# Performance work log

Hardware: AMD Instinct MI355X
Metric: run time of the kernel (lower is better)

The kernel has to match this reference:

```python
import jax, jax.numpy as jnp
import numpy as np

B, T, C = 2, 1024, 2048
NH, NKV = 16, 4
HD = C // NH          # 128
NUM_REP = NH // NKV   # 4


def _apply_rotation(x, angles):
    # x: (B, T, nh, hd); angles: (T, hd//2). Equivalent to the per-pair 2x2
    # rotation matmuls in the torch code: [x0', x1'] = [[cos,-sin],[sin,cos]] @ [x0, x1]
    Bx, Tx, nh, hd = x.shape
    xp = x.reshape(Bx, Tx, nh, hd // 2, 2)
    cos = jnp.cos(angles)[None, :, None, :]  # (1, T, 1, hd//2)
    sin = jnp.sin(angles)[None, :, None, :]
    x0, x1 = xp[..., 0], xp[..., 1]
    rot = jnp.stack([cos * x0 - sin * x1, sin * x0 + cos * x1], axis=-1)
    return rot.reshape(Bx, Tx, nh, hd)


def setup_inputs() -> dict:
    key = jax.random.key(0)
    ks = jax.random.split(key, 5)
    x = jax.random.normal(ks[0], (B, T, C), dtype=jnp.float32)
    # standard RoPE angle table: pos * 10000^(-2i/hd), shape (T, hd//2)
    inv_freq = 1.0 / (10000.0 ** (jnp.arange(0, HD, 2, dtype=jnp.float32) / HD))
    angles = jnp.arange(T, dtype=jnp.float32)[:, None] * inv_freq[None, :]
    s = 0.02
    wq = jax.random.normal(ks[1], (C, C), dtype=jnp.float32) * s
    wk = jax.random.normal(ks[2], (C, NKV * HD), dtype=jnp.float32) * s
    wv = jax.random.normal(ks[3], (C, NKV * HD), dtype=jnp.float32) * s
    wo = jax.random.normal(ks[4], (C, C), dtype=jnp.float32) * s
    return {"x": x, "angles": angles, "wq": wq, "wk": wk, "wv": wv, "wo": wo}


def reference(x, angles, wq, wk, wv, wo):
    Bx, Tx, Cx = x.shape
    q = (x @ wq).reshape(Bx, Tx, NH, HD)
    k = (x @ wk).reshape(Bx, Tx, NKV, HD)
    v = (x @ wv).reshape(Bx, Tx, NKV, HD)
    q = _apply_rotation(q, angles)
    k = _apply_rotation(k, angles)
    q = q.transpose(0, 2, 1, 3)  # (B, nh, T, hd)
    k = k.transpose(0, 2, 1, 3)  # (B, nkv, T, hd)
    v = v.transpose(0, 2, 1, 3)
    if NKV != 1:
        # torch .repeat tiles kv heads: query head h uses kv head h % NKV
        k = jnp.tile(k, (1, NUM_REP, 1, 1))
        v = jnp.tile(v, (1, NUM_REP, 1, 1))
    # Faithful quirks of the source: scores = K @ Q^T (keys on rows), NO 1/sqrt(hd) scale
    scores = jnp.einsum('bhkd,bhqd->bhkq', k, q)  # (B, nh, T, T)
    mask = jnp.triu(jnp.full((Tx, Tx), -jnp.inf, dtype=scores.dtype), k=1)
    scores = scores + mask
    w = jax.nn.softmax(scores, axis=-1)
    out = jnp.einsum('bhij,bhjd->bhid', w, v)   # (B, nh, T, hd)
    out = out.transpose(0, 2, 1, 3).reshape(Bx, Tx, Cx)
    return out @ wo
```

## Files before the change

kernel.cpp:

```cpp
#include <hip/hip_runtime.h>
#include <hip/hip_bf16.h>
#include <math.h>

#define BB 2
#define TT 1024
#define CC 2048
#define NH 16
#define NKV 4
#define HD 128
#define MROWS 2048
#define QKVN 3072
#define KOFF 2048
#define VOFF 2560

typedef unsigned short u16;
typedef unsigned int   u32;
typedef _Float16 f16;
typedef _Float16 f16x8 __attribute__((ext_vector_type(8)));
typedef short    s16x8 __attribute__((ext_vector_type(8)));
typedef float    f32x4 __attribute__((ext_vector_type(4)));

__device__ __forceinline__ u16 f2h(float f) {
    union { f16 h; u16 u; } x; x.h = (f16)f; return x.u;
}
__device__ __forceinline__ float h2f(u16 u) {
    union { u16 u; f16 h; } x; x.u = u; return (float)x.h;
}

#define GLDS(gp, lp) __builtin_amdgcn_global_load_lds( \
    (const __attribute__((address_space(1))) u32*)(gp), \
    (__attribute__((address_space(3))) u32*)(lp), 16, 0, 0)

__device__ __forceinline__ void wT_tile(const float* __restrict__ src,
                                        u16* __restrict__ Wt, int Nsrc,
                                        int row_off, int idx, int t,
                                        float tile[32][33]) {
    const int k0 = (idx & 63) * 32;
    const int n0 = (idx >> 6) * 32;
    const int r = t >> 3, c4 = (t & 7) * 4;
    float4 v = *(const float4*)&src[(size_t)(k0 + r) * Nsrc + n0 + c4];
    tile[r][c4 + 0] = v.x; tile[r][c4 + 1] = v.y;
    tile[r][c4 + 2] = v.z; tile[r][c4 + 3] = v.w;
    __syncthreads();
    ushort4 o;
    o.x = f2h(tile[c4 + 0][r]); o.y = f2h(tile[c4 + 1][r]);
    o.z = f2h(tile[c4 + 2][r]); o.w = f2h(tile[c4 + 3][r]);
    *(ushort4*)&Wt[(size_t)(row_off + n0 + r) * 2048 + k0 + c4] = o;
}

__global__ __launch_bounds__(256) void prep(const float* __restrict__ x,
                                            const float* __restrict__ wq,
                                            const float* __restrict__ wk,
                                            const float* __restrict__ wv,
                                            const float* __restrict__ wo,
                                            const float* __restrict__ angles,
                                            u16* __restrict__ xb,
                                            u16* __restrict__ Wt1,
                                            u16* __restrict__ Wt2,
                                            float2* __restrict__ cs) {
    __shared__ float tile[32][33];
    const int bid = blockIdx.x, t = threadIdx.x;
    if (bid < 4096) {
        int i = bid * 256 + t;
        float4 v = ((const float4*)x)[i];
        ushort4 o;
        o.x = f2h(v.x); o.y = f2h(v.y); o.z = f2h(v.z); o.w = f2h(v.w);
        ((ushort4*)xb)[i] = o;
    } else if (bid < 8192) {
        wT_tile(wq, Wt1, 2048, 0,    bid - 4096, t, tile);
    } else if (bid < 9216) {
        wT_tile(wk, Wt1, 512,  2048, bid - 8192, t, tile);
    } else if (bid < 10240) {
        wT_tile(wv, Wt1, 512,  2560, bid - 9216, t, tile);
    } else if (bid < 14336) {
        wT_tile(wo, Wt2, 2048, 0,    bid - 10240, t, tile);
    } else {
        int i = (bid - 14336) * 256 + t;
        float a = angles[i];
        cs[i] = make_float2(cosf(a), sinf(a));
    }
}

__global__ __launch_bounds__(256) void gemm_qkv(const u16* __restrict__ A,
                                                const u16* __restrict__ Bt,
                                                u16* __restrict__ qkv,
                                                u16* __restrict__ vtg,
                                                const float2* __restrict__ cs) {
    __shared__ __align__(16) u16 As0[128 * 64];
    __shared__ __align__(16) u16 As1[128 * 64];
    __shared__ __align__(16) u16 Bs0[96 * 64];
    __shared__ __align__(16) u16 Bs1[96 * 64];
    const int t = threadIdx.x, l = t & 63, w = t >> 6;
    const int row0 = blockIdx.y * 128;
    const int col0 = blockIdx.x * 96;
    const int wr = w >> 1, wc = w & 1;
    const int lg = l >> 4, ll = l & 15;
    const int K = 2048;

    f32x4 acc[4][3] = {};

#define QSTAGE(AS, BS, k0v) do {                                              \
    _Pragma("unroll")                                                         \
    for (int e_ = 0; e_ < 4; ++e_) {                                          \
        int r_ = 32 * w + 8 * e_ + (l >> 3);                                  \
        int cg_ = (l & 7) ^ (r_ & 7);                                         \
        GLDS(A + (size_t)(row0 + r_) * K + (k0v) + cg_ * 8,                   \
             (AS) + (32 * w + 8 * e_) * 64);                                  \
    }                                                                         \
    _Pragma("unroll")                                                         \
    for (int e_ = 0; e_ < 3; ++e_) {                                          \
        int r_ = 24 * w + 8 * e_ + (l >> 3);                                  \
        int cg_ = (l & 7) ^ (r_ & 7);                                         \
        GLDS(Bt + (size_t)(col0 + r_) * K + (k0v) + cg_ * 8,                  \
             (BS) + (24 * w + 8 * e_) * 64);                                  \
    }                                                                         \
} while (0)

#define QCOMP(AS, BS) do {                                                    \
    _Pragma("unroll")                                                         \
    for (int kc_ = 0; kc_ < 2; ++kc_) {                                       \
        f16x8 af_[4], bf_[3];                                                 \
        _Pragma("unroll")                                                     \
        for (int m_ = 0; m_ < 4; ++m_) {                                      \
            int row_ = wr * 64 + 16 * m_ + ll;                                \
            af_[m_] = *(const f16x8*)&(AS)[row_ * 64 +                        \
                        (((lg + 4 * kc_) ^ (ll & 7)) * 8)];                   \
        }                                                                     \
        _Pragma("unroll")                                                     \
        for (int n_ = 0; n_ < 3; ++n_) {                                      \
            int col_ = wc * 48 + 16 * n_ + ll;                                \
            bf_[n_] = *(const f16x8*)&(BS)[col_ * 64 +                        \
                        (((lg + 4 * kc_) ^ (ll & 7)) * 8)];                   \
        }                                                                     \
        _Pragma("unroll")                                                     \
        for (int m_ = 0; m_ < 4; ++m_)                                        \
            _Pragma("unroll")                                                 \
            for (int n_ = 0; n_ < 3; ++n_)                                    \
                acc[m_][n_] = __builtin_amdgcn_mfma_f32_16x16x32_f16(         \
                    af_[m_], bf_[n_], acc[m_][n_], 0, 0, 0);                  \
    }                                                                         \
} while (0)

    QSTAGE(As0, Bs0, 0);
    __syncthreads();
#pragma unroll 1
    for (int i = 0; i < 32; i += 2) {
        QSTAGE(As1, Bs1, (i + 1) * 64);
        QCOMP(As0, Bs0);
        __syncthreads();
        if (i + 2 < 32) QSTAGE(As0, Bs0, (i + 2) * 64);
        QCOMP(As1, Bs1);
        __syncthreads();
    }
#undef QSTAGE
#undef QCOMP

    const int orow = row0 + wr * 64 + lg * 4;
    const int ocol = col0 + wc * 48 + ll;
#pragma unroll
    for (int n = 0; n < 3; ++n) {
        const int col = ocol + 16 * n;
        if (col < VOFF) {
            const int p = (col & 127) >> 1;
            const bool odd = ll & 1;
#pragma unroll
            for (int m = 0; m < 4; ++m) {
#pragma unroll
                for (int r = 0; r < 4; ++r) {
                    float v = acc[m][n][r];
                    float pr = __shfl_xor(v, 1);
                    int row = orow + 16 * m + r;
                    float2 a = cs[(row & (TT - 1)) * 64 + p];
                    float res = odd ? (a.y * pr + a.x * v) : (a.x * v - a.y * pr);
                    qkv[(size_t)row * QKVN + col] = f2h(res);
                }
            }
        } else {
            int d = col - VOFF;
            const int hk = d >> 7; d &= 127;
            const int bb = orow >> 10;
            const int base_j = orow & (TT - 1);
#pragma unroll
            for (int m = 0; m < 4; ++m) {
                ushort4 pk;
                pk.x = f2h(acc[m][n][0]); pk.y = f2h(acc[m][n][1]);
                pk.z = f2h(acc[m][n][2]); pk.w = f2h(acc[m][n][3]);
                *(ushort4*)&vtg[((size_t)(bb * NKV + hk) * 128 + d) * 1024 + base_j + 16 * m] = pk;
            }
        }
    }
}

__global__ __launch_bounds__(256) void gemm_out(const u16* __restrict__ A,
                                                const u16* __restrict__ Bt,
                                                u16* __restrict__ Cb) {
    __shared__ __align__(16) u16 As0[128 * 64];
    __shared__ __align__(16) u16 As1[128 * 64];
    __shared__ __align__(16) u16 Bs0[128 * 64];
    __shared__ __align__(16) u16 Bs1[128 * 64];
    const int t = threadIdx.x, l = t & 63, w = t >> 6;
    const int row0 = blockIdx.y * 128;
    const int col0 = blockIdx.x * 128;
    const int koff = blockIdx.z * 1024;
    const int wr = w >> 1, wc = w & 1;
    const int lg = l >> 4, ll = l & 15;
    const int K = 2048;

    f32x4 acc[4][4] = {};

#define GSTAGE(AS, BS, k0v) do {                                              \
    _Pragma("unroll")                                                         \
    for (int e_ = 0; e_ < 4; ++e_) {                                          \
        int r_ = 32 * w + 8 * e_ + (l >> 3);                                  \
        int cg_ = (l & 7) ^ (r_ & 7);                                         \
        GLDS(A  + (size_t)(row0 + r_) * K + (k0v) + cg_ * 8,                  \
             (AS) + (32 * w + 8 * e_) * 64);                                  \
        GLDS(Bt + (size_t)(col0 + r_) * K + (k0v) + cg_ * 8,                  \
             (BS) + (32 * w + 8 * e_) * 64);                                  \
    }                                                                         \
} while (0)

#define GCOMP(AS, BS) do {                                                    \
    _Pragma("unroll")                                                         \
    for (int kc_ = 0; kc_ < 2; ++kc_) {                                       \
        f16x8 af_[4], bf_[4];                                                 \
        _Pragma("unroll")                                                     \
        for (int m_ = 0; m_ < 4; ++m_) {                                      \
            int row_ = wr * 64 + 16 * m_ + ll;                                \
            af_[m_] = *(const f16x8*)&(AS)[row_ * 64 +                        \
                        (((lg + 4 * kc_) ^ (ll & 7)) * 8)];                   \
            int col_ = wc * 64 + 16 * m_ + ll;                                \
            bf_[m_] = *(const f16x8*)&(BS)[col_ * 64 +                        \
                        (((lg + 4 * kc_) ^ (ll & 7)) * 8)];                   \
        }                                                                     \
        _Pragma("unroll")                                                     \
        for (int m_ = 0; m_ < 4; ++m_)                                        \
            _Pragma("unroll")                                                 \
            for (int n_ = 0; n_ < 4; ++n_)                                    \
                acc[m_][n_] = __builtin_amdgcn_mfma_f32_16x16x32_f16(         \
                    af_[m_], bf_[n_], acc[m_][n_], 0, 0, 0);                  \
    }                                                                         \
} while (0)

    GSTAGE(As0, Bs0, koff);
    __syncthreads();
#pragma unroll 1
    for (int i = 0; i < 16; i += 2) {
        GSTAGE(As1, Bs1, koff + (i + 1) * 64);
        GCOMP(As0, Bs0);
        __syncthreads();
        if (i + 2 < 16) GSTAGE(As0, Bs0, koff + (i + 2) * 64);
        GCOMP(As1, Bs1);
        __syncthreads();
    }
#undef GSTAGE
#undef GCOMP

    const size_t zoff = (size_t)blockIdx.z * MROWS * CC;
    const int orow = row0 + wr * 64 + lg * 4;
    const int ocol = col0 + wc * 64 + ll;
#pragma unroll
    for (int m = 0; m < 4; ++m)
#pragma unroll
        for (int nn = 0; nn < 4; ++nn)
#pragma unroll
            for (int r = 0; r < 4; ++r)
                Cb[zoff + (size_t)(orow + 16 * m + r) * CC + ocol + 16 * nn] =
                    f2h(acc[m][nn][r]);
}

__global__ void red_out(const u16* __restrict__ pp, float* __restrict__ out, int n8) {
    int i = blockIdx.x * 256 + threadIdx.x;
    if (i >= n8) return;
    const size_t PSZ = (size_t)MROWS * CC;
    s16x8 a = ((const s16x8*)pp)[i];
    s16x8 b = ((const s16x8*)(pp + PSZ))[i];
    float4 o0, o1;
    o0.x = h2f((u16)a[0]) + h2f((u16)b[0]);
    o0.y = h2f((u16)a[1]) + h2f((u16)b[1]);
    o0.z = h2f((u16)a[2]) + h2f((u16)b[2]);
    o0.w = h2f((u16)a[3]) + h2f((u16)b[3]);
    o1.x = h2f((u16)a[4]) + h2f((u16)b[4]);
    o1.y = h2f((u16)a[5]) + h2f((u16)b[5]);
    o1.z = h2f((u16)a[6]) + h2f((u16)b[6]);
    o1.w = h2f((u16)a[7]) + h2f((u16)b[7]);
    ((float4*)out)[2 * i]     = o0;
    ((float4*)out)[2 * i + 1] = o1;
}

__global__ __launch_bounds__(256) void attn_mfma(const u16* __restrict__ qkv,
                                                 const u16* __restrict__ vtg,
                                                 u16* __restrict__ attnb) {
    __shared__ __align__(16) u16 Qs0[64 * 128];
    __shared__ __align__(16) u16 Qs1[64 * 128];
    __shared__ __align__(16) u16 Vt0[128 * 64];
    __shared__ __align__(16) u16 Vt1[128 * 64];
    __shared__ __align__(16) u16 Ps[4 * 16 * 72];

    const int t = threadIdx.x, l = t & 63, w = t >> 6;
    const int bh = blockIdx.y;
    const int b = bh >> 4, h = bh & 15, hk = h & 3;
    const int lg = l >> 4, ll = l & 15;

    const u16* qbase = qkv + (size_t)(b * TT) * QKVN + h * 128;
    const u16* vbase = vtg + (size_t)((b * NKV + hk) * 128) * 1024;

    const int rq = 16 * w + (l >> 4);
    const int cq = l & 15;
    const int dv = 32 * w + (l >> 3);
    const int cv = l & 7;

#define STAGE(j0v, Qd, Vd) do {                                               \
    _Pragma("unroll")                                                         \
    for (int e_ = 0; e_ < 4; ++e_) {                                          \
        int r_ = rq + 4 * e_;                                                 \
        GLDS(qbase + (size_t)((j0v) + r_) * QKVN + ((cq ^ (r_ & 7)) * 8),     \
             (Qd) + (16 * w + 4 * e_) * 128);                                 \
    }                                                                         \
    _Pragma("unroll")                                                         \
    for (int e_ = 0; e_ < 4; ++e_) {                                          \
        int d_ = dv + 8 * e_;                                                 \
        GLDS(vbase + (size_t)d_ * 1024 + (j0v) + ((cv ^ (d_ & 7)) * 8),       \
             (Vd) + (32 * w + 8 * e_) * 64);                                  \
    }                                                                         \
} while (0)

#pragma unroll 1
    for (int ph = 0; ph < 2; ++ph) {
        const int it = ph ? (15 - blockIdx.x) : blockIdx.x;
        const int iw = it * 64 + w * 16;

        f16x8 kf[4];
        {
            const u16* kp = qkv + (size_t)(b * TT + iw + ll) * QKVN + KOFF + hk * 128 + lg * 8;
#pragma unroll
            for (int c = 0; c < 4; ++c) kf[c] = *(const f16x8*)(kp + 32 * c);
        }

        f32x4 o[8] = {};
        float mrun[4] = {-1e30f, -1e30f, -1e30f, -1e30f};
        float lrun[4] = {0.f, 0.f, 0.f, 0.f};

        const int nt = it + 1;
        STAGE(0, Qs0, Vt0);
        __syncthreads();

#pragma unroll 1
        for (int jt = 0; jt < nt; ++jt) {
            u16* Qc = (jt & 1) ? Qs1 : Qs0;
            u16* Vc = (jt & 1) ? Vt1 : Vt0;
            if (jt + 1 < nt) {
                u16* Qn = (jt & 1) ? Qs0 : Qs1;
                u16* Vn = (jt & 1) ? Vt0 : Vt1;
                STAGE((jt + 1) * 64, Qn, Vn);
            }

            f32x4 s[4] = {};
#pragma unroll
            for (int kc = 0; kc < 4; ++kc)
#pragma unroll
                for (int n = 0; n < 4; ++n) {
                    f16x8 qf = *(const f16x8*)&Qc[(16 * n + ll) * 128 + (((lg + 4 * kc) ^ (ll & 7)) * 8)];
                    s[n] = __builtin_amdgcn_mfma_f32_16x16x32_f16(kf[kc], qf, s[n], 0, 0, 0);
                }

            if (jt == it) {
#pragma unroll
                for (int n = 0; n < 4; ++n)
#pragma unroll
                    for (int r = 0; r < 4; ++r)
                        s[n][r] = (16 * n + ll <= 16 * w + 4 * lg + r) ? s[n][r] : -1e30f;
            }

            float tml[4];
            bool need = false;
#pragma unroll
            for (int r = 0; r < 4; ++r) {
                float tm = fmaxf(fmaxf(s[0][r], s[1][r]), fmaxf(s[2][r], s[3][r]));
                tml[r] = tm;
                need |= (tm > mrun[r] + 8.0f);
            }
            if (__any(need)) {
#pragma unroll
                for (int r = 0; r < 4; ++r) {
                    float tm = tml[r];
                    tm = fmaxf(tm, __shfl_xor(tm, 1, 16));
                    tm = fmaxf(tm, __shfl_xor(tm, 2, 16));
                    tm = fmaxf(tm, __shfl_xor(tm, 4, 16));
                    tm = fmaxf(tm, __shfl_xor(tm, 8, 16));
                    float mnew = fmaxf(mrun[r], tm);
                    float al = __expf(mrun[r] - mnew);
                    lrun[r] *= al;
                    mrun[r] = mnew;
#pragma unroll
                    for (int n = 0; n < 8; ++n) o[n][r] *= al;
                }
            }
            float p[4][4];
#pragma unroll
            for (int r = 0; r < 4; ++r) {
                float ps = 0.f;
#pragma unroll
                for (int n = 0; n < 4; ++n) { p[n][r] = __expf(s[n][r] - mrun[r]); ps += p[n][r]; }
                lrun[r] += ps;
            }

            u16* pw = Ps + w * (16 * 72);
#pragma unroll
            for (int n = 0; n < 4; ++n)
#pragma unroll
                for (int r = 0; r < 4; ++r)
                    pw[(4 * lg + r) * 72 + ll + 16 * n] = f2h(p[n][r]);
            f16x8 pa0 = *(const f16x8*)&pw[ll * 72 + 8 * lg];
            f16x8 pa1 = *(const f16x8*)&pw[ll * 72 + 8 * lg + 32];

#pragma unroll
            for (int n = 0; n < 8; ++n) {
                f16x8 vf0 = *(const f16x8*)&Vc[(16 * n + ll) * 64 + ((lg ^ (ll & 7)) * 8)];
                o[n] = __builtin_amdgcn_mfma_f32_16x16x32_f16(pa0, vf0, o[n], 0, 0, 0);
                f16x8 vf1 = *(const f16x8*)&Vc[(16 * n + ll) * 64 + (((lg + 4) ^ (ll & 7)) * 8)];
                o[n] = __builtin_amdgcn_mfma_f32_16x16x32_f16(pa1, vf1, o[n], 0, 0, 0);
            }

            __syncthreads();
        }

        u16* dst = attnb + (size_t)(b * TT + iw + 4 * lg) * CC + h * 128 + ll;
#pragma unroll
        for (int r = 0; r < 4; ++r) {
            float L = lrun[r];
            L += __shfl_xor(L, 1, 16);
            L += __shfl_xor(L, 2, 16);
            L += __shfl_xor(L, 4, 16);
            L += __shfl_xor(L, 8, 16);
            float inv = 1.0f / L;
#pragma unroll
            for (int n = 0; n < 8; ++n)
                dst[(size_t)r * CC + 16 * n] = f2h(o[n][r] * inv);
        }
    }
#undef STAGE
}

extern "C" void kernel_launch(void* const* d_in, const int* in_sizes, int n_in,
                              void* d_out, int out_size, void* d_ws, size_t ws_size,
                              hipStream_t stream) {
    const float* x      = (const float*)d_in[0];
    const float* angles = (const float*)d_in[1];
    const float* wq     = (const float*)d_in[2];
    const float* wk     = (const float*)d_in[3];
    const float* wv     = (const float*)d_in[4];
    const float* wo     = (const float*)d_in[5];
    float* out = (float*)d_out;

    char* ws = (char*)d_ws;
    u16*    Wt1   = (u16*)ws;
    u16*    Wt2   = (u16*)(ws + 12582912);
    float2* cs    = (float2*)(ws + 20971520);
    u16*    xb    = (u16*)(ws + 21495808);
    u16*    qkvb  = (u16*)(ws + 29884416);
    u16*    vtg   = (u16*)(ws + 42467328);
    u16*    attnb = (u16*)(ws + 44564480);
    u16*    p01   = (u16*)(ws + 21495808);

    prep<<<14592, 256, 0, stream>>>(x, wq, wk, wv, wo, angles, xb, Wt1, Wt2, cs);
    gemm_qkv<<<dim3(32, 16), 256, 0, stream>>>(xb, Wt1, qkvb, vtg, cs);
    attn_mfma<<<dim3(8, BB * NH), 256, 0, stream>>>(qkvb, vtg, attnb);
    gemm_out<<<dim3(16, 16, 2), 256, 0, stream>>>(attnb, Wt2, p01);
    red_out<<<2048, 256, 0, stream>>>(p01, out, MROWS * CC / 8);
}
```

Before: 125.3 us.

## Drop split-K in output GEMM and write fp32 directly with 8 waves

The output projection no longer splits K across two blocks with fp16 partial buffers and a separate reduction kernel. Each 128x128 tile now runs the full K=2048 loop with 512 threads (8 waves, each computing 64x32) and stores fp32 results straight to the output. This removes a kernel launch, the partial-sum round trip through memory, and the fp16 rounding of partials. In exchange the grid has half as many blocks (256), and each block runs a K loop twice as long.

```diff
diff --git a/kernel.cpp b/kernel.cpp
--- a/kernel.cpp
+++ b/kernel.cpp
@@ -191,9 +191,9 @@
     }
 }
 
-__global__ __launch_bounds__(256) void gemm_out(const u16* __restrict__ A,
+__global__ __launch_bounds__(512) void gemm_out(const u16* __restrict__ A,
                                                 const u16* __restrict__ Bt,
-                                                u16* __restrict__ Cb) {
+                                                float* __restrict__ Cf) {
     __shared__ __align__(16) u16 As0[128 * 64];
     __shared__ __align__(16) u16 As1[128 * 64];
     __shared__ __align__(16) u16 Bs0[128 * 64];
@@ -201,91 +201,73 @@
     const int t = threadIdx.x, l = t & 63, w = t >> 6;
     const int row0 = blockIdx.y * 128;
     const int col0 = blockIdx.x * 128;
-    const int koff = blockIdx.z * 1024;
-    const int wr = w >> 1, wc = w & 1;
+    const int wr = w >> 2, wc = w & 3;
     const int lg = l >> 4, ll = l & 15;
     const int K = 2048;
 
-    f32x4 acc[4][4] = {};
+    f32x4 acc[4][2] = {};
 
 #define GSTAGE(AS, BS, k0v) do {                                              \
     _Pragma("unroll")                                                         \
-    for (int e_ = 0; e_ < 4; ++e_) {                                          \
-        int r_ = 32 * w + 8 * e_ + (l >> 3);                                  \
+    for (int e_ = 0; e_ < 2; ++e_) {                                          \
+        int r_ = 16 * w + 8 * e_ + (l >> 3);                                  \
         int cg_ = (l & 7) ^ (r_ & 7);                                         \
         GLDS(A  + (size_t)(row0 + r_) * K + (k0v) + cg_ * 8,                  \
-             (AS) + (32 * w + 8 * e_) * 64);                                  \
+             (AS) + (16 * w + 8 * e_) * 64);                                  \
         GLDS(Bt + (size_t)(col0 + r_) * K + (k0v) + cg_ * 8,                  \
-             (BS) + (32 * w + 8 * e_) * 64);                                  \
+             (BS) + (16 * w + 8 * e_) * 64);                                  \
     }                                                                         \
 } while (0)
 
 #define GCOMP(AS, BS) do {                                                    \
     _Pragma("unroll")                                                         \
     for (int kc_ = 0; kc_ < 2; ++kc_) {                                       \
-        f16x8 af_[4], bf_[4];                                                 \
+        f16x8 af_[4], bf_[2];                                                 \
         _Pragma("unroll")                                                     \
         for (int m_ = 0; m_ < 4; ++m_) {                                      \
             int row_ = wr * 64 + 16 * m_ + ll;                                \
             af_[m_] = *(const f16x8*)&(AS)[row_ * 64 +                        \
                         (((lg + 4 * kc_) ^ (ll & 7)) * 8)];                   \
-            int col_ = wc * 64 + 16 * m_ + ll;                                \
-            bf_[m_] = *(const f16x8*)&(BS)[col_ * 64 +                        \
+        }                                                                     \
+        _Pragma("unroll")                                                     \
+        for (int n_ = 0; n_ < 2; ++n_) {                                      \
+            int col_ = wc * 32 + 16 * n_ + ll;                                \
+            bf_[n_] = *(const f16x8*)&(BS)[col_ * 64 +                        \
                         (((lg + 4 * kc_) ^ (ll & 7)) * 8)];                   \
         }                                                                     \
         _Pragma("unroll")                                                     \
         for (int m_ = 0; m_ < 4; ++m_)                                        \
             _Pragma("unroll")                                                 \
-            for (int n_ = 0; n_ < 4; ++n_)                                    \
+            for (int n_ = 0; n_ < 2; ++n_)                                    \
                 acc[m_][n_] = __builtin_amdgcn_mfma_f32_16x16x32_f16(         \
                     af_[m_], bf_[n_], acc[m_][n_], 0, 0, 0);                  \
     }                                                                         \
 } while (0)
 
-    GSTAGE(As0, Bs0, koff);
+    GSTAGE(As0, Bs0, 0);
     __syncthreads();
 #pragma unroll 1
-    for (int i = 0; i < 16; i += 2) {
-        GSTAGE(As1, Bs1, koff + (i + 1) * 64);
+    for (int i = 0; i < 32; i += 2) {
+        GSTAGE(As1, Bs1, (i + 1) * 64);
         GCOMP(As0, Bs0);
         __syncthreads();
-        if (i + 2 < 16) GSTAGE(As0, Bs0, koff + (i + 2) * 64);
+        if (i + 2 < 32) GSTAGE(As0, Bs0, (i + 2) * 64);
         GCOMP(As1, Bs1);
         __syncthreads();
     }
 #undef GSTAGE
 #undef GCOMP
 
-    const size_t zoff = (size_t)blockIdx.z * MROWS * CC;
     const int orow = row0 + wr * 64 + lg * 4;
-    const int ocol = col0 + wc * 64 + ll;
+    const int ocol = col0 + wc * 32 + ll;
 #pragma unroll
     for (int m = 0; m < 4; ++m)
 #pragma unroll
-        for (int nn = 0; nn < 4; ++nn)
+        for (int nn = 0; nn < 2; ++nn)
 #pragma unroll
             for (int r = 0; r < 4; ++r)
-                Cb[zoff + (size_t)(orow + 16 * m + r) * CC + ocol + 16 * nn] =
-                    f2h(acc[m][nn][r]);
-}
-
-__global__ void red_out(const u16* __restrict__ pp, float* __restrict__ out, int n8) {
-    int i = blockIdx.x * 256 + threadIdx.x;
-    if (i >= n8) return;
-    const size_t PSZ = (size_t)MROWS * CC;
-    s16x8 a = ((const s16x8*)pp)[i];
-    s16x8 b = ((const s16x8*)(pp + PSZ))[i];
-    float4 o0, o1;
-    o0.x = h2f((u16)a[0]) + h2f((u16)b[0]);
-    o0.y = h2f((u16)a[1]) + h2f((u16)b[1]);
-    o0.z = h2f((u16)a[2]) + h2f((u16)b[2]);
-    o0.w = h2f((u16)a[3]) + h2f((u16)b[3]);
-    o1.x = h2f((u16)a[4]) + h2f((u16)b[4]);
-    o1.y = h2f((u16)a[5]) + h2f((u16)b[5]);
-    o1.z = h2f((u16)a[6]) + h2f((u16)b[6]);
-    o1.w = h2f((u16)a[7]) + h2f((u16)b[7]);
-    ((float4*)out)[2 * i]     = o0;
-    ((float4*)out)[2 * i + 1] = o1;
+                Cf[(size_t)(orow + 16 * m + r) * CC + ocol + 16 * nn] =
+                    acc[m][nn][r];
 }
 
 __global__ __launch_bounds__(256) void attn_mfma(const u16* __restrict__ qkv,
@@ -461,11 +443,9 @@
     u16*    qkvb  = (u16*)(ws + 29884416);
     u16*    vtg   = (u16*)(ws + 42467328);
     u16*    attnb = (u16*)(ws + 44564480);
-    u16*    p01   = (u16*)(ws + 21495808);
 
     prep<<<14592, 256, 0, stream>>>(x, wq, wk, wv, wo, angles, xb, Wt1, Wt2, cs);
     gemm_qkv<<<dim3(32, 16), 256, 0, stream>>>(xb, Wt1, qkvb, vtg, cs);
     attn_mfma<<<dim3(8, BB * NH), 256, 0, stream>>>(qkvb, vtg, attnb);
-    gemm_out<<<dim3(16, 16, 2), 256, 0, stream>>>(attnb, Wt2, p01);
-    red_out<<<2048, 256, 0, stream>>>(p01, out, MROWS * CC / 8);
-}
+    gemm_out<<<dim3(16, 16), 512, 0, stream>>>(attnb, Wt2, out);
+}
```

Result: faster. 116.7 us (-6.8%).
